# Kernel optimization log

Hardware: AMD Instinct MI355X
Metric: run time of the kernel (lower is better)

## Reference

```python
import jax, jax.numpy as jnp
import numpy as np
from jax import lax

# Faithful JAX port of the approxmatch CUDA kernel (Fan et al. EMD):
#   iterates annealing levels j = 7 .. -2 with level = -4^j (0 at j=-2),
#   alternately normalizing transport weights by remaining source capacity
#   (remainL) and capping by remaining target capacity (remainR).
# Cost = sum over matched pairs of Euclidean (sqrt) distance * match weight.

def _approx_match(xyz1, xyz2):
    # xyz1: (b,n,3), xyz2: (b,m,3)
    b, n, _ = xyz1.shape
    m = xyz2.shape[1]
    # squared pairwise distances (b,n,m) -- computed once, reused every level
    d2 = jnp.sum((xyz1[:, :, None, :] - xyz2[:, None, :, :]) ** 2, axis=-1)
    # CUDA kernel capacities: multiL = max(1, m/n), multiR = max(1, n/m) (int ratios)
    multiL = float(max(1, m // n))
    multiR = float(max(1, n // m))
    remainL = jnp.full((b, n), multiL, dtype=xyz1.dtype)
    remainR = jnp.full((b, m), multiR, dtype=xyz1.dtype)
    match = jnp.zeros((b, n, m), dtype=xyz1.dtype)

    # levels for j = 7..-1 are -4^j; j = -2 uses level = 0
    levels = jnp.concatenate([
        -(4.0 ** jnp.arange(7, -2, -1, dtype=jnp.float32)),
        jnp.zeros((1,), jnp.float32),
    ])

    def body(carry, level):
        match, remainL, remainR = carry
        w = jnp.exp(level * d2) * remainR[:, None, :]                 # (b,n,m)
        w = w * (remainL / (1e-9 + w.sum(axis=2)))[:, :, None]        # normalize rows, scale by L capacity
        r = jnp.minimum(remainR / (1e-9 + w.sum(axis=1)), 1.0)        # cap columns by R capacity
        w = w * r[:, None, :]
        match = match + w
        remainL = jnp.maximum(remainL - w.sum(axis=2), 0.0)
        remainR = jnp.maximum(remainR - w.sum(axis=1), 0.0)
        return (match, remainL, remainR), None

    (match, _, _), _ = lax.scan(body, (match, remainL, remainR), levels)
    return match, d2


def _match_cost(match, d2):
    # matchcost kernel: sum_{k,l} match[k,l] * sqrt(||xyz1_k - xyz2_l||^2)
    dist = jnp.sqrt(jnp.maximum(d2, 1e-30))
    return jnp.sum(match * dist, axis=(1, 2))  # (b,)


def setup_inputs() -> dict:
    key = jax.random.key(0)
    k1, k2 = jax.random.split(key)
    b, n, m = 8, 2048, 2048
    input1 = jax.random.uniform(k1, (b, n, 3), dtype=jnp.float32)
    input2 = jax.random.uniform(k2, (b, m, 3), dtype=jnp.float32)
    return {"input1": input1, "input2": input2}


def reference(input1, input2):
    match, d2 = _approx_match(input1, input2)
    return _match_cost(match, d2)  # (b,) per-batch EMD cost
```

## Files before the change

kernel.cpp:

```cpp
#include <hip/hip_runtime.h>
#include <math.h>


#define NPTS 2048
#define BLOCK 256
#define RPB 16
#define L2E 1.4426950408889634f

typedef float v2 __attribute__((ext_vector_type(2)));

__device__ __forceinline__ float fexp2(float x) { return __builtin_amdgcn_exp2f(x); }
__device__ __forceinline__ float fsqrt(float x) { return __builtin_amdgcn_sqrtf(x); }
__device__ __forceinline__ float flog2(float x) { return __builtin_amdgcn_logf(x); }
__device__ __forceinline__ v2 fma2(v2 a, v2 b, v2 c) { return __builtin_elementwise_fma(a, b, c); }
__device__ __forceinline__ v2 sp(float a) { v2 r; r.x = a; r.y = a; return r; }
__device__ __forceinline__ float xreduce(float v) {
#pragma unroll
    for (int off = 1; off < 64; off <<= 1) v += __shfl_xor(v, off, 64);
    return v;
}

struct RowPair { v2 pa, px, py, pz; };
__device__ __forceinline__ RowPair mk_pair(float4 a, float4 b, float kp) {
    RowPair r;
    r.pa = v2{kp * a.w, kp * b.w};
    r.px = v2{-2.f*kp*a.x, -2.f*kp*b.x};
    r.py = v2{-2.f*kp*a.y, -2.f*kp*b.y};
    r.pz = v2{-2.f*kp*a.z, -2.f*kp*b.z};
    return r;
}
__device__ __forceinline__ v2 term(const RowPair& r, float qx, float qy, float qz, v2 qb2) {
    return fma2(r.px, sp(qx), fma2(r.py, sp(qy), fma2(r.pz, sp(qz), r.pa + qb2)));
}
__device__ __forceinline__ float4 with_sq(float4 p) {
    p.w = p.x*p.x + p.y*p.y + p.z*p.z;
    return p;
}

__global__ __launch_bounds__(BLOCK) void k_A(
    const float* __restrict__ xyz1, const float* __restrict__ xyz2,
    float4* __restrict__ p1w, float4* __restrict__ p2w,
    float* __restrict__ f_g, float kk, float multiL, float multiR)
{
    __shared__ float4 sQ[NPTS];
    const int row0 = blockIdx.x * RPB;
    const int batch = row0 >> 11;
    const int rloc = row0 & 2047;
    const float* g1 = xyz1 + (size_t)batch * NPTS * 3;
    const float* g2 = xyz2 + (size_t)batch * NPTS * 3;
    if (threadIdx.x < RPB) {
        int i = rloc + threadIdx.x;
        p1w[((size_t)batch << 11) + i] = make_float4(g1[3*i], g1[3*i+1], g1[3*i+2], 0.f);
    } else if (threadIdx.x < 2 * RPB) {
        int i = rloc + threadIdx.x - RPB;
        p2w[((size_t)batch << 11) + i] = make_float4(g2[3*i], g2[3*i+1], g2[3*i+2], 0.f);
    }
    for (int j = threadIdx.x; j < NPTS; j += BLOCK) {
        float qx = g2[3*j], qy = g2[3*j+1], qz = g2[3*j+2];
        sQ[j] = make_float4(qx, qy, qz, kk * (qx*qx + qy*qy + qz*qz));
    }
    __syncthreads();
    const int lane = threadIdx.x & 63;
    const int wave = threadIdx.x >> 6;
    const int r0 = row0 + wave * 4;
    RowPair rA, rB;
    {
        const float* p = g1 + 3 * (r0 & 2047);
        float4 p0 = make_float4(p[0], p[1], p[2], p[0]*p[0]+p[1]*p[1]+p[2]*p[2]);
        float4 p1 = make_float4(p[3], p[4], p[5], p[3]*p[3]+p[4]*p[4]+p[5]*p[5]);
        float4 p2 = make_float4(p[6], p[7], p[8], p[6]*p[6]+p[7]*p[7]+p[8]*p[8]);
        float4 p3 = make_float4(p[9], p[10], p[11], p[9]*p[9]+p[10]*p[10]+p[11]*p[11]);
        rA = mk_pair(p0, p1, kk); rB = mk_pair(p2, p3, kk);
    }
    v2 aSA = sp(0.f), aSB = sp(0.f);
#pragma unroll 8
    for (int j = lane; j < NPTS; j += 64) {
        float4 q = sQ[j];
        v2 qb2 = sp(q.w);
        v2 tA = term(rA, q.x, q.y, q.z, qb2);
        v2 tB = term(rB, q.x, q.y, q.z, qb2);
        aSA += v2{fexp2(tA.x), fexp2(tA.y)};
        aSB += v2{fexp2(tB.x), fexp2(tB.y)};
    }
    float sv[4] = {xreduce(aSA.x), xreduce(aSA.y), xreduce(aSB.x), xreduce(aSB.y)};
    if (lane == 0) {
#pragma unroll
        for (int r = 0; r < 4; ++r)
            f_g[r0 + r] = multiL / (1e-9f + multiR * sv[r]);
    }
}

template <bool FIRST>
__global__ __launch_bounds__(BLOCK) void k_B(
    const float4* __restrict__ p1w, const float4* __restrict__ p2w,
    const float* __restrict__ f_g, float* __restrict__ remR,
    float* __restrict__ c_g, float kk, float multiR)
{
    __shared__ float4 sQ[NPTS];
    const int col0 = blockIdx.x * RPB;
    const int batch = col0 >> 11;
    const float4* P1 = p1w + ((size_t)batch << 11);
    const float* F = f_g + ((size_t)batch << 11);
    for (int i = threadIdx.x; i < NPTS; i += BLOCK) {
        float4 q = P1[i];
        q.w = kk * (q.x*q.x + q.y*q.y + q.z*q.z) + flog2(F[i]);
        sQ[i] = q;
    }
    __syncthreads();
    const int lane = threadIdx.x & 63;
    const int wave = threadIdx.x >> 6;
    const int c0 = col0 + wave * 4;
    RowPair rA, rB;
    {
        float4 q0 = with_sq(p2w[c0]),     q1 = with_sq(p2w[c0+1]);
        float4 q2 = with_sq(p2w[c0+2]),   q3 = with_sq(p2w[c0+3]);
        rA = mk_pair(q0, q1, kk); rB = mk_pair(q2, q3, kk);
    }
    v2 aSA = sp(0.f), aSB = sp(0.f);
#pragma unroll 8
    for (int i = lane; i < NPTS; i += 64) {
        float4 p = sQ[i];
        v2 qb2 = sp(p.w);
        v2 tA = term(rA, p.x, p.y, p.z, qb2);
        v2 tB = term(rB, p.x, p.y, p.z, qb2);
        aSA += v2{fexp2(tA.x), fexp2(tA.y)};
        aSB += v2{fexp2(tB.x), fexp2(tB.y)};
    }
    float sv[4] = {xreduce(aSA.x), xreduce(aSA.y), xreduce(aSB.x), xreduce(aSB.y)};
    if (lane == 0) {
#pragma unroll
        for (int r = 0; r < 4; ++r) {
            int gj = c0 + r;
            float R = FIRST ? multiR : remR[gj];
            float colsum = R * sv[r];
            float rr = fminf(R / (1e-9f + colsum), 1.0f);
            c_g[gj] = R * rr;
            remR[gj] = fmaxf(R - colsum * rr, 0.f);
        }
    }
}

__global__ __launch_bounds__(BLOCK) void k_B9(
    const float* __restrict__ f_g, const float* __restrict__ remR,
    float* __restrict__ c_g, float* __restrict__ out)
{
    __shared__ float wsum[BLOCK / 64];
    const int batch = blockIdx.x;
    const float* F = f_g + ((size_t)batch << 11);
    float s = 0.f;
    for (int i = threadIdx.x; i < NPTS; i += BLOCK) s += F[i];
    s = xreduce(s);
    int wave = threadIdx.x >> 6, lane = threadIdx.x & 63;
    if (lane == 0) wsum[wave] = s;
    __syncthreads();
    float Ftot = (wsum[0] + wsum[1]) + (wsum[2] + wsum[3]);
    if (threadIdx.x == 0) out[batch] = 0.f;
    for (int j = threadIdx.x; j < NPTS; j += BLOCK) {
        int gj = (batch << 11) + j;
        float R = remR[gj];
        float colsum = R * Ftot;
        float rr = fminf(R / (1e-9f + colsum), 1.0f);
        c_g[gj] = R * rr;
    }
}

template <int MODE, bool FIRSTC>
__global__ __launch_bounds__(BLOCK) void k_CA(
    const float4* __restrict__ p1w, const float4* __restrict__ p2w,
    float* __restrict__ f_g, const float* __restrict__ c_g,
    const float* __restrict__ remR, float* __restrict__ remL,
    float* __restrict__ costrow, float kp, float rsqkp, float multiL)
{
    __shared__ float4 sQ[NPTS];
    __shared__ float2 sCR[NPTS];
    const int row0 = blockIdx.x * RPB;
    const int batch = row0 >> 11;
    const float4* P2 = p2w + ((size_t)batch << 11);
    const float* C = c_g + ((size_t)batch << 11);
    const float* R = remR + ((size_t)batch << 11);
    for (int j = threadIdx.x; j < NPTS; j += BLOCK) {
        float4 q = P2[j];
        q.w = kp * (q.x*q.x + q.y*q.y + q.z*q.z);
        sQ[j] = q;
        sCR[j] = make_float2(C[j], R[j]);
    }
    __syncthreads();
    const int lane = threadIdx.x & 63;
    const int wave = threadIdx.x >> 6;
    const int r0 = row0 + wave * 4;

    RowPair rA, rB;
    v2 fiA, fiB;
    {
        float4 p0 = with_sq(p1w[r0]),   p1 = with_sq(p1w[r0+1]);
        float4 p2 = with_sq(p1w[r0+2]), p3 = with_sq(p1w[r0+3]);
        rA = mk_pair(p0, p1, kp); rB = mk_pair(p2, p3, kp);
        fiA = v2{f_g[r0], f_g[r0+1]}; fiB = v2{f_g[r0+2], f_g[r0+3]};
    }
    v2 aTA = sp(0.f), aTB = sp(0.f), aUA = sp(0.f), aUB = sp(0.f);
    v2 aAA = sp(0.f), aAB = sp(0.f);
    float aAs = 0.f;
#pragma unroll 4
    for (int j = lane; j < NPTS; j += 64) {
        float4 q = sQ[j];
        float2 crj = sCR[j];
        v2 qb2 = sp(q.w);
        float cw = crj.x, rw = crj.y;
        v2 tA = term(rA, q.x, q.y, q.z, qb2);
        v2 tB = term(rB, q.x, q.y, q.z, qb2);
        v2 eA = v2{fexp2(tA.x), fexp2(tA.y)};
        v2 eB = v2{fexp2(tB.x), fexp2(tB.y)};
        v2 eCA, eCB;
        if (MODE == 1) {
            v2 e2A = eA * eA, e2B = eB * eB;
            eCA = sp(cw) * (e2A * e2A); eCB = sp(cw) * (e2B * e2B);
        } else {
            eCA = sp(cw) * eA; eCB = sp(cw) * eB;
        }
        aTA += eCA; aTB += eCB;
        v2 stA = v2{fsqrt(fabsf(tA.x)), fsqrt(fabsf(tA.y))};
        v2 stB = v2{fsqrt(fabsf(tB.x)), fsqrt(fabsf(tB.y))};
        aUA = fma2(eCA, stA, aUA); aUB = fma2(eCB, stB, aUB);
        if (MODE == 1) { aAA = fma2(sp(rw), eA, aAA); aAB = fma2(sp(rw), eB, aAB); }
        else           { aAs += rw; }
    }
    float aas = (MODE == 2) ? xreduce(aAs) : 0.f;
    float tt[4] = {xreduce(aTA.x), xreduce(aTA.y), xreduce(aTB.x), xreduce(aTB.y)};
    float uu[4] = {xreduce(aUA.x), xreduce(aUA.y), xreduce(aUB.x), xreduce(aUB.y)};
    float aav[4];
    if (MODE == 1) {
        aav[0] = xreduce(aAA.x); aav[1] = xreduce(aAA.y);
        aav[2] = xreduce(aAB.x); aav[3] = xreduce(aAB.y);
    } else {
        aav[0] = aav[1] = aav[2] = aav[3] = aas;
    }
    float fiv[4] = {fiA.x, fiA.y, fiB.x, fiB.y};
    if (lane == 0) {
#pragma unroll
        for (int r = 0; r < 4; ++r) {
            int gi = r0 + r;
            float rl0 = FIRSTC ? multiL : remL[gi];
            float rl = fmaxf(rl0 - fiv[r] * tt[r], 0.f);
            costrow[gi] = (FIRSTC ? 0.f : costrow[gi]) + fiv[r] * uu[r] * rsqkp;
            remL[gi] = rl;
            f_g[gi] = rl / (1e-9f + aav[r]);
        }
    }
}

__global__ __launch_bounds__(BLOCK) void k_C9(
    const float4* __restrict__ p1w, const float4* __restrict__ p2w,
    const float* __restrict__ f_g, const float* __restrict__ c_g,
    const float* __restrict__ costrow, float* __restrict__ out)
{
    __shared__ float4 sQ[NPTS];
    __shared__ float sC[NPTS];
    __shared__ float wsum[BLOCK / 64];
    const int row0 = blockIdx.x * RPB;
    const int batch = row0 >> 11;
    const float4* P2 = p2w + ((size_t)batch << 11);
    const float* C = c_g + ((size_t)batch << 11);
    for (int j = threadIdx.x; j < NPTS; j += BLOCK) {
        sQ[j] = P2[j];
        sC[j] = C[j];
    }
    __syncthreads();
    const int lane = threadIdx.x & 63;
    const int wave = threadIdx.x >> 6;
    const int r0 = row0 + wave * 4;
    float px[4], py[4], pz[4], aU[4];
#pragma unroll
    for (int r = 0; r < 4; ++r) {
        float4 q = p1w[r0 + r];
        px[r] = q.x; py[r] = q.y; pz[r] = q.z; aU[r] = 0.f;
    }
#pragma unroll 4
    for (int j = lane; j < NPTS; j += 64) {
        float4 q = sQ[j];
        float cw = sC[j];
#pragma unroll
        for (int r = 0; r < 4; ++r) {
            float dx = px[r]-q.x, dy = py[r]-q.y, dz = pz[r]-q.z;
            float d2 = fmaf(dx, dx, fmaf(dy, dy, dz * dz));
            aU[r] = fmaf(cw, fsqrt(d2), aU[r]);
        }
    }
    float psum = 0.f;
#pragma unroll
    for (int r = 0; r < 4; ++r) {
        float uu = xreduce(aU[r]);
        if (lane == 0) psum += costrow[r0 + r] + f_g[r0 + r] * uu;
    }
    if (lane == 0) wsum[wave] = psum;
    __syncthreads();
    if (threadIdx.x == 0)
        atomicAdd(&out[batch], (wsum[0] + wsum[1]) + (wsum[2] + wsum[3]));
}

extern "C" void kernel_launch(void* const* d_in, const int* in_sizes, int n_in,
                              void* d_out, int out_size, void* d_ws, size_t ws_size,
                              hipStream_t stream) {
    const float* xyz1 = (const float*)d_in[0];
    const float* xyz2 = (const float*)d_in[1];
    float* out = (float*)d_out;
    const int b = out_size;
    const int n = in_sizes[0] / (3 * b);
    const int m = in_sizes[1] / (3 * b);
    const int bn = b * n, bm = b * m;

    float4* p1w = (float4*)d_ws;
    float4* p2w = p1w + bn;
    float* remL    = (float*)(p2w + bm);
    float* remR    = remL + bn;
    float* f       = remR + bm;
    float* c       = f + bn;
    float* costrow = c + bm;

    const float multiL = (float)((m / n > 1) ? (m / n) : 1);
    const float multiR = (float)((n / m > 1) ? (n / m) : 1);

    dim3 g(bn / RPB), blk(BLOCK);
    const float kk0 = -16384.f * L2E;
    k_A<<<g, blk, 0, stream>>>(xyz1, xyz2, p1w, p2w, f, kk0, multiL, multiR);

    for (int t = 0; t < 9; ++t) {
        const float kk = -exp2f(2.f * (float)(7 - t)) * L2E;
        if (t == 0)
            k_B<true><<<g, blk, 0, stream>>>(p1w, p2w, f, remR, c, kk, multiR);
        else
            k_B<false><<<g, blk, 0, stream>>>(p1w, p2w, f, remR, c, kk, multiR);

        if (t < 8) {
            const float kp = kk * 0.25f;
            const float rsq = 1.f / sqrtf(-kp);
            if (t == 0)
                k_CA<1, true><<<g, blk, 0, stream>>>(p1w, p2w, f, c, remR, remL,
                                                     costrow, kp, rsq, multiL);
            else
                k_CA<1, false><<<g, blk, 0, stream>>>(p1w, p2w, f, c, remR, remL,
                                                      costrow, kp, rsq, multiL);
        } else {
            const float kp = -0.25f * L2E;
            const float rsq = 1.f / sqrtf(0.25f * L2E);
            k_CA<2, false><<<g, blk, 0, stream>>>(p1w, p2w, f, c, remR, remL,
                                                  costrow, kp, rsq, multiL);
        }
    }
    k_B9<<<dim3(b), blk, 0, stream>>>(f, remR, c, out);
    k_C9<<<g, blk, 0, stream>>>(p1w, p2w, f, c, costrow, out);
}
```

Baseline: 276.2 us.

## Morton-sort points and skip far chunks via bounding-box exponent cutoff

A new per-batch kernel sorts both point clouds by a 3D Morton code using a shared-memory bitonic sort. It stores the sorted points with their squared norms and writes per-64-point bounding boxes. The A, B and CA kernels then compute a box-to-box gap distance for each 64-point chunk and skip chunks whose minimum squared distance times the annealing coefficient puts the exp2 argument below the float underflow range. This aims to cut most of the exp and sqrt work at the sharp early levels. In exchange it adds a sort kernel, more workspace, and a branchy, non-unrolled inner loop that loses instruction-level parallelism at the later levels where little can be skipped.

```diff
diff --git a/kernel.cpp b/kernel.cpp
--- a/kernel.cpp
+++ b/kernel.cpp
@@ -32,50 +32,126 @@
 __device__ __forceinline__ v2 term(const RowPair& r, float qx, float qy, float qz, v2 qb2) {
     return fma2(r.px, sp(qx), fma2(r.py, sp(qy), fma2(r.pz, sp(qz), r.pa + qb2)));
 }
-__device__ __forceinline__ float4 with_sq(float4 p) {
-    p.w = p.x*p.x + p.y*p.y + p.z*p.z;
-    return p;
-}
-
-__global__ __launch_bounds__(BLOCK) void k_A(
+
+__device__ __forceinline__ void bbox16(const float4* __restrict__ p, int start, int lane,
+                                       float& lx, float& ly, float& lz,
+                                       float& hx, float& hy, float& hz) {
+    float4 q = p[start + (lane & 15)];
+    lx = q.x; hx = q.x; ly = q.y; hy = q.y; lz = q.z; hz = q.z;
+#pragma unroll
+    for (int off = 1; off < 16; off <<= 1) {
+        lx = fminf(lx, __shfl_xor(lx, off, 64));
+        hx = fmaxf(hx, __shfl_xor(hx, off, 64));
+        ly = fminf(ly, __shfl_xor(ly, off, 64));
+        hy = fmaxf(hy, __shfl_xor(hy, off, 64));
+        lz = fminf(lz, __shfl_xor(lz, off, 64));
+        hz = fmaxf(hz, __shfl_xor(hz, off, 64));
+    }
+}
+
+__device__ __forceinline__ unsigned spread3(unsigned v) {
+    v &= 0x3FFu;
+    v = (v | (v << 16)) & 0x030000FFu;
+    v = (v | (v << 8))  & 0x0300F00Fu;
+    v = (v | (v << 4))  & 0x030C30C3u;
+    v = (v | (v << 2))  & 0x09249249u;
+    return v;
+}
+
+__global__ __launch_bounds__(256) void k_sort(
     const float* __restrict__ xyz1, const float* __restrict__ xyz2,
     float4* __restrict__ p1w, float4* __restrict__ p2w,
-    float* __restrict__ f_g, float kk, float multiL, float multiR)
+    float4* __restrict__ bb1, float4* __restrict__ bb2)
+{
+    __shared__ float sx[NPTS], sy[NPTS], sz[NPTS];
+    __shared__ unsigned skey[NPTS];
+    const int batch = blockIdx.x >> 1;
+    const int side  = blockIdx.x & 1;
+    const float* src = (side ? xyz2 : xyz1) + (size_t)batch * NPTS * 3;
+    float4* dst = (side ? p2w : p1w) + ((size_t)batch << 11);
+    float4* bb  = (side ? bb2 : bb1) + batch * 64;
+    const int tid = threadIdx.x;
+    for (int i = tid; i < NPTS; i += 256) {
+        float x = src[3*i], y = src[3*i+1], z = src[3*i+2];
+        sx[i] = x; sy[i] = y; sz[i] = z;
+        int cx = (int)(x * 128.f); cx = cx < 0 ? 0 : (cx > 127 ? 127 : cx);
+        int cy = (int)(y * 128.f); cy = cy < 0 ? 0 : (cy > 127 ? 127 : cy);
+        int cz = (int)(z * 128.f); cz = cz < 0 ? 0 : (cz > 127 ? 127 : cz);
+        unsigned m = (spread3((unsigned)cx) << 2) | (spread3((unsigned)cy) << 1)
+                   | spread3((unsigned)cz);
+        skey[i] = (m << 11) | (unsigned)i;
+    }
+    for (unsigned k = 2; k <= NPTS; k <<= 1) {
+        for (unsigned j = k >> 1; j > 0; j >>= 1) {
+            __syncthreads();
+            for (int i = tid; i < NPTS; i += 256) {
+                int l = i ^ (int)j;
+                if (l > i) {
+                    unsigned a = skey[i], b = skey[l];
+                    bool up = ((i & (int)k) == 0);
+                    if ((a > b) == up) { skey[i] = b; skey[l] = a; }
+                }
+            }
+        }
+    }
+    __syncthreads();
+    for (int i = tid; i < NPTS; i += 256) {
+        unsigned idx = skey[i] & 2047u;
+        float x = sx[idx], y = sy[idx], z = sz[idx];
+        dst[i] = make_float4(x, y, z, x*x + y*y + z*z);
+    }
+    const int wave = tid >> 6, lane = tid & 63;
+    for (int c = wave; c < 32; c += 4) {
+        unsigned idx = skey[c * 64 + lane] & 2047u;
+        float x = sx[idx], y = sy[idx], z = sz[idx];
+        float lx=x,hx=x,ly=y,hy=y,lz=z,hz=z;
+#pragma unroll
+        for (int off = 1; off < 64; off <<= 1) {
+            lx = fminf(lx, __shfl_xor(lx, off, 64));
+            hx = fmaxf(hx, __shfl_xor(hx, off, 64));
+            ly = fminf(ly, __shfl_xor(ly, off, 64));
+            hy = fmaxf(hy, __shfl_xor(hy, off, 64));
+            lz = fminf(lz, __shfl_xor(lz, off, 64));
+            hz = fmaxf(hz, __shfl_xor(hz, off, 64));
+        }
+        if (lane == 0) {
+            bb[2*c]   = make_float4(lx, ly, lz, 0.f);
+            bb[2*c+1] = make_float4(hx, hy, hz, 0.f);
+        }
+    }
+}
+
+__global__ __launch_bounds__(BLOCK) void k_A(
+    const float4* __restrict__ p1w, const float4* __restrict__ p2w,
+    const float4* __restrict__ bb2, float* __restrict__ f_g,
+    float kk, float cutd2, float multiL, float multiR)
 {
     __shared__ float4 sQ[NPTS];
+    __shared__ float4 sBB[64];
     const int row0 = blockIdx.x * RPB;
     const int batch = row0 >> 11;
-    const int rloc = row0 & 2047;
-    const float* g1 = xyz1 + (size_t)batch * NPTS * 3;
-    const float* g2 = xyz2 + (size_t)batch * NPTS * 3;
-    if (threadIdx.x < RPB) {
-        int i = rloc + threadIdx.x;
-        p1w[((size_t)batch << 11) + i] = make_float4(g1[3*i], g1[3*i+1], g1[3*i+2], 0.f);
-    } else if (threadIdx.x < 2 * RPB) {
-        int i = rloc + threadIdx.x - RPB;
-        p2w[((size_t)batch << 11) + i] = make_float4(g2[3*i], g2[3*i+1], g2[3*i+2], 0.f);
-    }
+    const float4* P2 = p2w + ((size_t)batch << 11);
     for (int j = threadIdx.x; j < NPTS; j += BLOCK) {
-        float qx = g2[3*j], qy = g2[3*j+1], qz = g2[3*j+2];
-        sQ[j] = make_float4(qx, qy, qz, kk * (qx*qx + qy*qy + qz*qz));
-    }
+        float4 q = P2[j]; q.w *= kk; sQ[j] = q;
+    }
+    if (threadIdx.x < 64) sBB[threadIdx.x] = bb2[batch * 64 + threadIdx.x];
     __syncthreads();
     const int lane = threadIdx.x & 63;
     const int wave = threadIdx.x >> 6;
     const int r0 = row0 + wave * 4;
-    RowPair rA, rB;
-    {
-        const float* p = g1 + 3 * (r0 & 2047);
-        float4 p0 = make_float4(p[0], p[1], p[2], p[0]*p[0]+p[1]*p[1]+p[2]*p[2]);
-        float4 p1 = make_float4(p[3], p[4], p[5], p[3]*p[3]+p[4]*p[4]+p[5]*p[5]);
-        float4 p2 = make_float4(p[6], p[7], p[8], p[6]*p[6]+p[7]*p[7]+p[8]*p[8]);
-        float4 p3 = make_float4(p[9], p[10], p[11], p[9]*p[9]+p[10]*p[10]+p[11]*p[11]);
-        rA = mk_pair(p0, p1, kk); rB = mk_pair(p2, p3, kk);
-    }
+    RowPair rA = mk_pair(p1w[r0],   p1w[r0+1], kk);
+    RowPair rB = mk_pair(p1w[r0+2], p1w[r0+3], kk);
+    float lx, ly, lz, hx, hy, hz;
+    bbox16(p1w, row0, lane, lx, ly, lz, hx, hy, hz);
     v2 aSA = sp(0.f), aSB = sp(0.f);
-#pragma unroll 8
-    for (int j = lane; j < NPTS; j += 64) {
-        float4 q = sQ[j];
+#pragma unroll 1
+    for (int it = 0; it < NPTS / 64; ++it) {
+        float4 blo = sBB[2*it], bhi = sBB[2*it+1];
+        float gx = fmaxf(fmaxf(blo.x - hx, lx - bhi.x), 0.f);
+        float gy = fmaxf(fmaxf(blo.y - hy, ly - bhi.y), 0.f);
+        float gz = fmaxf(fmaxf(blo.z - hz, lz - bhi.z), 0.f);
+        if (fmaf(gx, gx, fmaf(gy, gy, gz * gz)) > cutd2) continue;
+        float4 q = sQ[it * 64 + lane];
         v2 qb2 = sp(q.w);
         v2 tA = term(rA, q.x, q.y, q.z, qb2);
         v2 tB = term(rB, q.x, q.y, q.z, qb2);
@@ -90,36 +166,44 @@
     }
 }
 
-template <bool FIRST>
+template <bool FIRST, bool SKIP>
 __global__ __launch_bounds__(BLOCK) void k_B(
     const float4* __restrict__ p1w, const float4* __restrict__ p2w,
-    const float* __restrict__ f_g, float* __restrict__ remR,
-    float* __restrict__ c_g, float kk, float multiR)
+    const float4* __restrict__ bb1, const float* __restrict__ f_g,
+    float* __restrict__ remR, float* __restrict__ c_g,
+    float kk, float cutd2, float multiR)
 {
     __shared__ float4 sQ[NPTS];
+    __shared__ float4 sBB[64];
     const int col0 = blockIdx.x * RPB;
     const int batch = col0 >> 11;
     const float4* P1 = p1w + ((size_t)batch << 11);
     const float* F = f_g + ((size_t)batch << 11);
     for (int i = threadIdx.x; i < NPTS; i += BLOCK) {
         float4 q = P1[i];
-        q.w = kk * (q.x*q.x + q.y*q.y + q.z*q.z) + flog2(F[i]);
+        q.w = kk * q.w + flog2(F[i]);
         sQ[i] = q;
     }
+    if (threadIdx.x < 64) sBB[threadIdx.x] = bb1[batch * 64 + threadIdx.x];
     __syncthreads();
     const int lane = threadIdx.x & 63;
     const int wave = threadIdx.x >> 6;
     const int c0 = col0 + wave * 4;
-    RowPair rA, rB;
-    {
-        float4 q0 = with_sq(p2w[c0]),     q1 = with_sq(p2w[c0+1]);
-        float4 q2 = with_sq(p2w[c0+2]),   q3 = with_sq(p2w[c0+3]);
-        rA = mk_pair(q0, q1, kk); rB = mk_pair(q2, q3, kk);
-    }
+    RowPair rA = mk_pair(p2w[c0],   p2w[c0+1], kk);
+    RowPair rB = mk_pair(p2w[c0+2], p2w[c0+3], kk);
+    float lx, ly, lz, hx, hy, hz;
+    bbox16(p2w, col0, lane, lx, ly, lz, hx, hy, hz);
     v2 aSA = sp(0.f), aSB = sp(0.f);
-#pragma unroll 8
-    for (int i = lane; i < NPTS; i += 64) {
-        float4 p = sQ[i];
+#pragma unroll 1
+    for (int it = 0; it < NPTS / 64; ++it) {
+        if (SKIP) {
+            float4 blo = sBB[2*it], bhi = sBB[2*it+1];
+            float gx = fmaxf(fmaxf(blo.x - hx, lx - bhi.x), 0.f);
+            float gy = fmaxf(fmaxf(blo.y - hy, ly - bhi.y), 0.f);
+            float gz = fmaxf(fmaxf(blo.z - hz, lz - bhi.z), 0.f);
+            if (fmaf(gx, gx, fmaf(gy, gy, gz * gz)) > cutd2) continue;
+        }
+        float4 p = sQ[it * 64 + lane];
         v2 qb2 = sp(p.w);
         v2 tA = term(rA, p.x, p.y, p.z, qb2);
         v2 tB = term(rB, p.x, p.y, p.z, qb2);
@@ -164,15 +248,17 @@
     }
 }
 
-template <int MODE, bool FIRSTC>
+template <int MODE, bool FIRSTC, bool SKIP>
 __global__ __launch_bounds__(BLOCK) void k_CA(
     const float4* __restrict__ p1w, const float4* __restrict__ p2w,
-    float* __restrict__ f_g, const float* __restrict__ c_g,
-    const float* __restrict__ remR, float* __restrict__ remL,
-    float* __restrict__ costrow, float kp, float rsqkp, float multiL)
+    const float4* __restrict__ bb2, float* __restrict__ f_g,
+    const float* __restrict__ c_g, const float* __restrict__ remR,
+    float* __restrict__ remL, float* __restrict__ costrow,
+    float kp, float rsqkp, float cutd2, float multiL)
 {
     __shared__ float4 sQ[NPTS];
     __shared__ float2 sCR[NPTS];
+    __shared__ float4 sBB[64];
     const int row0 = blockIdx.x * RPB;
     const int batch = row0 >> 11;
     const float4* P2 = p2w + ((size_t)batch << 11);
@@ -180,32 +266,38 @@
     const float* R = remR + ((size_t)batch << 11);
     for (int j = threadIdx.x; j < NPTS; j += BLOCK) {
         float4 q = P2[j];
-        q.w = kp * (q.x*q.x + q.y*q.y + q.z*q.z);
+        q.w *= kp;
         sQ[j] = q;
         sCR[j] = make_float2(C[j], R[j]);
     }
+    if (threadIdx.x < 64) sBB[threadIdx.x] = bb2[batch * 64 + threadIdx.x];
     __syncthreads();
     const int lane = threadIdx.x & 63;
     const int wave = threadIdx.x >> 6;
     const int r0 = row0 + wave * 4;
 
-    RowPair rA, rB;
-    v2 fiA, fiB;
-    {
-        float4 p0 = with_sq(p1w[r0]),   p1 = with_sq(p1w[r0+1]);
-        float4 p2 = with_sq(p1w[r0+2]), p3 = with_sq(p1w[r0+3]);
-        rA = mk_pair(p0, p1, kp); rB = mk_pair(p2, p3, kp);
-        fiA = v2{f_g[r0], f_g[r0+1]}; fiB = v2{f_g[r0+2], f_g[r0+3]};
-    }
+    RowPair rA = mk_pair(p1w[r0],   p1w[r0+1], kp);
+    RowPair rB = mk_pair(p1w[r0+2], p1w[r0+3], kp);
+    v2 fiA = v2{f_g[r0], f_g[r0+1]}, fiB = v2{f_g[r0+2], f_g[r0+3]};
+    float lx, ly, lz, hx, hy, hz;
+    bbox16(p1w, row0, lane, lx, ly, lz, hx, hy, hz);
     v2 aTA = sp(0.f), aTB = sp(0.f), aUA = sp(0.f), aUB = sp(0.f);
     v2 aAA = sp(0.f), aAB = sp(0.f);
     float aAs = 0.f;
-#pragma unroll 4
-    for (int j = lane; j < NPTS; j += 64) {
-        float4 q = sQ[j];
-        float2 crj = sCR[j];
+#pragma unroll 1
+    for (int it = 0; it < NPTS / 64; ++it) {
+        if (SKIP) {
+            float4 blo = sBB[2*it], bhi = sBB[2*it+1];
+            float gx = fmaxf(fmaxf(blo.x - hx, lx - bhi.x), 0.f);
+            float gy = fmaxf(fmaxf(blo.y - hy, ly - bhi.y), 0.f);
+            float gz = fmaxf(fmaxf(blo.z - hz, lz - bhi.z), 0.f);
+            if (fmaf(gx, gx, fmaf(gy, gy, gz * gz)) > cutd2) continue;
+        }
+        float4 q = sQ[it * 64 + lane];
+        float2 crj = sCR[it * 64 + lane];
         v2 qb2 = sp(q.w);
         float cw = crj.x, rw = crj.y;
+        if (MODE == 2) aAs += rw;
         v2 tA = term(rA, q.x, q.y, q.z, qb2);
         v2 tB = term(rB, q.x, q.y, q.z, qb2);
         v2 eA = v2{fexp2(tA.x), fexp2(tA.y)};
@@ -222,7 +314,6 @@
         v2 stB = v2{fsqrt(fabsf(tB.x)), fsqrt(fabsf(tB.y))};
         aUA = fma2(eCA, stA, aUA); aUB = fma2(eCB, stB, aUB);
         if (MODE == 1) { aAA = fma2(sp(rw), eA, aAA); aAB = fma2(sp(rw), eB, aAB); }
-        else           { aAs += rw; }
     }
     float aas = (MODE == 2) ? xreduce(aAs) : 0.f;
     float tt[4] = {xreduce(aTA.x), xreduce(aTA.y), xreduce(aTB.x), xreduce(aTB.y)};
@@ -315,35 +406,51 @@
     float* f       = remR + bm;
     float* c       = f + bn;
     float* costrow = c + bm;
+    float4* bb1    = (float4*)(costrow + bn);
+    float4* bb2    = bb1 + (size_t)b * 64;
 
     const float multiL = (float)((m / n > 1) ? (m / n) : 1);
     const float multiR = (float)((n / m > 1) ? (n / m) : 1);
 
     dim3 g(bn / RPB), blk(BLOCK);
-    const float kk0 = -16384.f * L2E;
-    k_A<<<g, blk, 0, stream>>>(xyz1, xyz2, p1w, p2w, f, kk0, multiL, multiR);
+    k_sort<<<dim3(2 * b), blk, 0, stream>>>(xyz1, xyz2, p1w, p2w, bb1, bb2);
+
+    const float absk0 = 16384.f * L2E;
+    k_A<<<g, blk, 0, stream>>>(p1w, p2w, bb2, f, -absk0, 152.f / absk0,
+                               multiL, multiR);
 
     for (int t = 0; t < 9; ++t) {
-        const float kk = -exp2f(2.f * (float)(7 - t)) * L2E;
+        const float abskk = exp2f(2.f * (float)(7 - t)) * L2E;
+        const float kk = -abskk;
+        const float cutB = 183.f / abskk;
         if (t == 0)
-            k_B<true><<<g, blk, 0, stream>>>(p1w, p2w, f, remR, c, kk, multiR);
+            k_B<true, true><<<g, blk, 0, stream>>>(p1w, p2w, bb1, f, remR, c,
+                                                   kk, cutB, multiR);
+        else if (cutB < 3.0f)
+            k_B<false, true><<<g, blk, 0, stream>>>(p1w, p2w, bb1, f, remR, c,
+                                                    kk, cutB, multiR);
         else
-            k_B<false><<<g, blk, 0, stream>>>(p1w, p2w, f, remR, c, kk, multiR);
+            k_B<false, false><<<g, blk, 0, stream>>>(p1w, p2w, bb1, f, remR, c,
+                                                     kk, cutB, multiR);
 
         if (t < 8) {
             const float kp = kk * 0.25f;
+            const float cutCA = 152.f / (abskk * 0.25f);
             const float rsq = 1.f / sqrtf(-kp);
             if (t == 0)
-                k_CA<1, true><<<g, blk, 0, stream>>>(p1w, p2w, f, c, remR, remL,
-                                                     costrow, kp, rsq, multiL);
+                k_CA<1, true, true><<<g, blk, 0, stream>>>(p1w, p2w, bb2, f, c,
+                    remR, remL, costrow, kp, rsq, cutCA, multiL);
+            else if (cutCA < 3.0f)
+                k_CA<1, false, true><<<g, blk, 0, stream>>>(p1w, p2w, bb2, f, c,
+                    remR, remL, costrow, kp, rsq, cutCA, multiL);
             else
-                k_CA<1, false><<<g, blk, 0, stream>>>(p1w, p2w, f, c, remR, remL,
-                                                      costrow, kp, rsq, multiL);
+                k_CA<1, false, false><<<g, blk, 0, stream>>>(p1w, p2w, bb2, f, c,
+                    remR, remL, costrow, kp, rsq, cutCA, multiL);
         } else {
             const float kp = -0.25f * L2E;
             const float rsq = 1.f / sqrtf(0.25f * L2E);
-            k_CA<2, false><<<g, blk, 0, stream>>>(p1w, p2w, f, c, remR, remL,
-                                                  costrow, kp, rsq, multiL);
+            k_CA<2, false, false><<<g, blk, 0, stream>>>(p1w, p2w, bb2, f, c,
+                remR, remL, costrow, kp, rsq, 1e30f, multiL);
         }
     }
     k_B9<<<dim3(b), blk, 0, stream>>>(f, remR, c, out);
```

Result: slower. 403.2 us (+46.0%).
